# Optimization experiments

Hardware: AMD Instinct MI355X
Metric: run time of the kernel (lower is better)

## Reference

```python
import math
import jax, jax.numpy as jnp
import numpy as np

N, MA, DESIGN, RADIAL, SOFTENING, RM = 8, 24, 26, 15, 3, 5.0


def setup_inputs() -> dict:
    key = jax.random.key(0)
    k1, k2 = jax.random.split(key, 2)
    # atomic coordinates, spread out so interatomic distances are realistic (bohr)
    coords = jax.random.normal(k1, (N, MA, 3), jnp.float32) * 3.0
    # labels all >= 0 -> full padding (padding[i] == MA for every molecule)
    labels = jax.random.randint(k2, (N, MA), 0, 10)
    # deterministic synthetic Lebedev-like design (26 points on the unit sphere)
    phi = jnp.linspace(0.0, 2.0 * math.pi, DESIGN, endpoint=False).astype(jnp.float32)
    psi = jnp.linspace(0.1, math.pi - 0.1, DESIGN).astype(jnp.float32)
    sphere = jnp.stack([jnp.cos(phi) * jnp.sin(psi),
                        jnp.sin(phi) * jnp.sin(psi),
                        jnp.cos(psi)], axis=1)           # [D, 3]
    sphere_weights = jnp.full((DESIGN,), 1.0 / DESIGN, dtype=jnp.float32)
    return {"labels": labels, "coords": coords,
            "sphere": sphere, "sphere_weights": sphere_weights}


def _spheric_grid(sphere, sphere_weights):
    # Gauss-Chebyshev radial quadrature mapped by the Becke transform
    i = jnp.arange(1, RADIAL + 1, dtype=jnp.float32)
    z = -jnp.cos(math.pi * (2.0 * i - 1.0) / (2.0 * RADIAL))
    dr = 2.0 * RM * (1.0 - z) ** -2
    r = RM * (1.0 + z) / (1.0 - z)
    w = jnp.sqrt(1.0 - z ** 2) * dr * math.pi / RADIAL
    w = r ** 2 * 4.0 * math.pi * w                       # [R]
    conc = (r[:, None, None] * sphere[None]).reshape(-1, 3)          # [R*D, 3]
    wt = (sphere_weights[None, :] * w[:, None]).reshape(-1)          # [R*D]
    return conc, wt


def _becke(x, r, dm, idx):
    # x [n, mx, 3] grid points, r [n, M, 3] centers, dm [n, M, M], idx [mx]
    rx = jnp.linalg.norm(x[:, :, None, :] - r[:, None, :, :], axis=-1)   # [n, mx, M]
    # elliptic coordinate mu_ij for every grid point: [n, mx, M, M]
    mu = (rx[..., :, None] - rx[..., None, :]) / jnp.clip(dm[:, None], 1e-12, None)
    for _ in range(1, SOFTENING):                       # softening passes
        mu = 0.5 * mu * (3.0 - mu ** 2)
    mu = 0.5 * (1.0 - mu)
    mu = mu + 0.5 * jnp.eye(dm.shape[-1], dtype=x.dtype)  # diagonal -> 1
    cell = jnp.prod(mu, axis=-1)                        # [n, mx, M] cell functions
    v_i = jnp.take_along_axis(cell, idx[None, :, None], axis=2)[..., 0]
    return v_i / cell.sum(axis=2)


def reference(labels, coords, sphere, sphere_weights):
    # labels are all >= 0 here, so padding == MA for every molecule and the
    # original per-molecule loop collapses into one batched computation.
    conc, wt = _spheric_grid(sphere, sphere_weights)    # conc [ms,3], wt [ms]
    ms = conc.shape[0]
    n, M, _ = coords.shape
    dm = jnp.linalg.norm(coords[:, :, None, :] - coords[:, None, :, :], axis=-1)
    # place concentric spheres on each atom (atom-major ordering, as in torch)
    grid = (coords[:, :, None, :] + conc[None, None]).reshape(n, M * ms, 3)
    w_full = jnp.broadcast_to(wt[None, :], (M, ms)).reshape(-1)      # [M*ms]
    idx = jnp.repeat(jnp.arange(M), ms)                              # sample -> center
    v = _becke(grid, coords, dm, idx)                                # [n, M*ms]
    weights = v * w_full[None, :]
    dv = grid[:, :, None, :] - coords[:, None, :, :]                 # [n, M*ms, M, 3]
    return grid, dv, weights
```

## Files before the change

kernel.cpp:

```cpp
#include <hip/hip_runtime.h>
#include <math.h>

constexpr int MAC = 24;
constexpr int DES = 26;
constexpr int RAD = 15;
constexpr int MS  = RAD * DES;
constexpr int MX  = MAC * MS;
constexpr int PPB = 8;
constexpr int BPM = MX / PPB;

__global__ __launch_bounds__(512) void becke_precompute(
    const float* __restrict__ coords, const float* __restrict__ sphere,
    const float* __restrict__ sw, int nmol,
    float* __restrict__ inv_dm, float* __restrict__ conc4, float* __restrict__ wt)
{
    __shared__ float rr[RAD], ww[RAD];
    const int tid = threadIdx.x;
    if (tid < RAD) {
        double i   = (double)tid + 1.0;
        double z   = -cos(M_PI * (2.0 * i - 1.0) / (2.0 * (double)RAD));
        double omz = 1.0 - z;
        double dr  = 10.0 / (omz * omz);
        double r   = 5.0 * (1.0 + z) / omz;
        double w1  = sqrt(1.0 - z * z) * dr * M_PI / (double)RAD;
        rr[tid] = (float)r;
        ww[tid] = (float)(r * r * 4.0 * M_PI * w1);
    }
    __syncthreads();
    for (int t = tid; t < MS; t += 512) {
        int k = t / DES, d = t - k * DES;
        conc4[t * 4 + 0] = rr[k] * sphere[d * 3 + 0];
        conc4[t * 4 + 1] = rr[k] * sphere[d * 3 + 1];
        conc4[t * 4 + 2] = rr[k] * sphere[d * 3 + 2];
        conc4[t * 4 + 3] = 0.0f;
        wt[t] = sw[d] * ww[k];
    }
    for (int e = tid; e < nmol * MAC * MAC; e += 512) {
        int n = e / (MAC * MAC), r0 = e - n * MAC * MAC;
        int i = r0 / MAC, j = r0 - i * MAC;
        const float* cb = coords + n * MAC * 3;
        float dx = cb[i * 3 + 0] - cb[j * 3 + 0];
        float dy = cb[i * 3 + 1] - cb[j * 3 + 1];
        float dz = cb[i * 3 + 2] - cb[j * 3 + 2];
        float dd = sqrtf(dx * dx + dy * dy + dz * dz);
        inv_dm[e] = 1.0f / fmaxf(dd, 1e-12f);
    }
}

__global__ __launch_bounds__(256) void becke_main(
    const float* __restrict__ coords,
    const float* __restrict__ inv_dm,
    const float* __restrict__ conc4,
    const float* __restrict__ wt,
    float* __restrict__ og,
    float* __restrict__ odv,
    float* __restrict__ ow)
{
    const int tid = threadIdx.x;
    const int l   = tid & 31;
    const int n   = blockIdx.x / BPM;
    const int sm  = (blockIdx.x - n * BPM) * PPB + (tid >> 5);
    const int a   = sm / MS;
    const int t   = sm - a * MS;
    const bool act = (l < MAC);
    const int  i   = act ? l : (MAC - 1);

    const float4 cc  = *reinterpret_cast<const float4*>(conc4 + t * 4);
    const float  wtt = wt[t];
    const float* cb  = coords + n * MAC * 3;

    const float gx = cb[a * 3 + 0] + cc.x;
    const float gy = cb[a * 3 + 1] + cc.y;
    const float gz = cb[a * 3 + 2] + cc.z;

    const float dx = gx - cb[i * 3 + 0];
    const float dy = gy - cb[i * 3 + 1];
    const float dz = gz - cb[i * 3 + 2];
    const size_t sg = (size_t)n * MX + sm;
    if (act) {
        float* dvp = odv + (sg * MAC + i) * 3;
        dvp[0] = dx; dvp[1] = dy; dvp[2] = dz;
    }
    const float rxi = sqrtf(dx * dx + dy * dy + dz * dz);

    float inv[MAC];
    const float* irow = inv_dm + (n * MAC + i) * MAC;
    #pragma unroll
    for (int q = 0; q < MAC / 4; ++q) {
        float4 v = *reinterpret_cast<const float4*>(irow + q * 4);
        inv[q * 4 + 0] = v.x; inv[q * 4 + 1] = v.y;
        inv[q * 4 + 2] = v.z; inv[q * 4 + 3] = v.w;
    }

    float prod = 1.0f;
    #pragma unroll
    for (int j = 0; j < MAC; ++j) {
        float rxj = __shfl(rxi, j, 32);
        float mu  = (rxi - rxj) * inv[j];
        mu *= fmaf(mu * mu, -0.5f, 1.5f);
        mu *= fmaf(mu * mu, -0.5f, 1.5f);
        prod *= fmaf(mu, -0.5f, 0.5f);
    }
    float cell = act ? (prod + prod) : 0.0f;

    float sum = cell;
    #pragma unroll
    for (int m = 16; m >= 1; m >>= 1) sum += __shfl_xor(sum, m, 32);
    const float ca = __shfl(cell, a, 32);

    if (l == MAC) {
        float* gp = og + sg * 3;
        gp[0] = gx; gp[1] = gy; gp[2] = gz;
    } else if (l == MAC + 1) {
        ow[sg] = (ca / sum) * wtt;
    }
}

extern "C" void kernel_launch(void* const* d_in, const int* in_sizes, int n_in,
                              void* d_out, int out_size, void* d_ws, size_t ws_size,
                              hipStream_t stream) {
    const float* coords = (const float*)d_in[1];
    const float* sphere = (const float*)d_in[2];
    const float* sw     = (const float*)d_in[3];

    const int nmol = in_sizes[1] / (MAC * 3);

    float* ws     = (float*)d_ws;
    float* inv_dm = ws;
    float* conc4  = inv_dm + (size_t)nmol * MAC * MAC;
    float* wtab   = conc4 + MS * 4;

    float* o     = (float*)d_out;
    float* ogrid = o;
    float* odv   = ogrid + (size_t)nmol * MX * 3;
    float* owt   = odv + (size_t)nmol * MX * MAC * 3;

    becke_precompute<<<dim3(1), dim3(512), 0, stream>>>(
        coords, sphere, sw, nmol, inv_dm, conc4, wtab);
    becke_main<<<dim3(nmol * BPM), dim3(256), 0, stream>>>(
        coords, inv_dm, conc4, wtab, ogrid, odv, owt);
}
```

Measured before the change: 84.06 us.

## Process four grid points per half-warp and parallelize precompute across blocks

Each 32-lane group now handles four sample points instead of one, so the per-atom inverse-distance row and atom coordinates loaded into registers are reused across four points. Broadcasts and reductions use ds_swizzle instead of generic shuffles, and the weight normalization uses a fast reciprocal. The precompute moves from one block to a multi-block grid, packs radial weights into the conc4 w component, and pads coords to float4. This trades higher register pressure and fewer blocks for less redundant loading and less launch serialization in the precompute.

```diff
diff --git a/kernel.cpp b/kernel.cpp
--- a/kernel.cpp
+++ b/kernel.cpp
@@ -1,41 +1,42 @@
 #include <hip/hip_runtime.h>
 #include <math.h>
+#include <type_traits>
 
 constexpr int MAC = 24;
 constexpr int DES = 26;
 constexpr int RAD = 15;
 constexpr int MS  = RAD * DES;
 constexpr int MX  = MAC * MS;
-constexpr int PPB = 8;
+constexpr int PPG = 4;
+constexpr int GPB = 6;
+constexpr int PPB = PPG * GPB;
 constexpr int BPM = MX / PPB;
 
-__global__ __launch_bounds__(512) void becke_precompute(
+template <int N, int I = 0, typename F>
+__device__ __forceinline__ void static_for(F&& f) {
+    if constexpr (I < N) {
+        f(std::integral_constant<int, I>{});
+        static_for<N, I + 1>(f);
+    }
+}
+
+template <int J>
+__device__ __forceinline__ float bcast32(float v) {
+    return __int_as_float(__builtin_amdgcn_ds_swizzle(__float_as_int(v), (J << 5)));
+}
+template <int M>
+__device__ __forceinline__ float xorswz(float v) {
+    return __int_as_float(__builtin_amdgcn_ds_swizzle(__float_as_int(v), (M << 10) | 0x1f));
+}
+
+__global__ __launch_bounds__(256) void becke_pre(
     const float* __restrict__ coords, const float* __restrict__ sphere,
     const float* __restrict__ sw, int nmol,
-    float* __restrict__ inv_dm, float* __restrict__ conc4, float* __restrict__ wt)
+    float* __restrict__ inv_dm, float4* __restrict__ conc4, float4* __restrict__ cpad)
 {
-    __shared__ float rr[RAD], ww[RAD];
-    const int tid = threadIdx.x;
-    if (tid < RAD) {
-        double i   = (double)tid + 1.0;
-        double z   = -cos(M_PI * (2.0 * i - 1.0) / (2.0 * (double)RAD));
-        double omz = 1.0 - z;
-        double dr  = 10.0 / (omz * omz);
-        double r   = 5.0 * (1.0 + z) / omz;
-        double w1  = sqrt(1.0 - z * z) * dr * M_PI / (double)RAD;
-        rr[tid] = (float)r;
-        ww[tid] = (float)(r * r * 4.0 * M_PI * w1);
-    }
-    __syncthreads();
-    for (int t = tid; t < MS; t += 512) {
-        int k = t / DES, d = t - k * DES;
-        conc4[t * 4 + 0] = rr[k] * sphere[d * 3 + 0];
-        conc4[t * 4 + 1] = rr[k] * sphere[d * 3 + 1];
-        conc4[t * 4 + 2] = rr[k] * sphere[d * 3 + 2];
-        conc4[t * 4 + 3] = 0.0f;
-        wt[t] = sw[d] * ww[k];
-    }
-    for (int e = tid; e < nmol * MAC * MAC; e += 512) {
+    const int e = blockIdx.x * 256 + threadIdx.x;
+    const int nidm = nmol * MAC * MAC;
+    if (e < nidm) {
         int n = e / (MAC * MAC), r0 = e - n * MAC * MAC;
         int i = r0 / MAC, j = r0 - i * MAC;
         const float* cb = coords + n * MAC * 3;
@@ -44,75 +45,126 @@
         float dz = cb[i * 3 + 2] - cb[j * 3 + 2];
         float dd = sqrtf(dx * dx + dy * dy + dz * dz);
         inv_dm[e] = 1.0f / fmaxf(dd, 1e-12f);
+        return;
+    }
+    const int e2 = e - nidm;
+    if (e2 < MS) {
+        int k = e2 / DES, d = e2 - k * DES;
+        double i   = (double)k + 1.0;
+        double z   = -cos(M_PI * (2.0 * i - 1.0) / (2.0 * (double)RAD));
+        double omz = 1.0 - z;
+        double dr  = 10.0 / (omz * omz);
+        double r   = 5.0 * (1.0 + z) / omz;
+        double w1  = sqrt(1.0 - z * z) * dr * M_PI / (double)RAD;
+        double w   = r * r * 4.0 * M_PI * w1;
+        conc4[e2] = make_float4((float)(r * (double)sphere[d * 3 + 0]),
+                                (float)(r * (double)sphere[d * 3 + 1]),
+                                (float)(r * (double)sphere[d * 3 + 2]),
+                                (float)((double)sw[d] * w));
+        return;
+    }
+    const int e3 = e2 - MS;
+    if (e3 < nmol * MAC) {
+        cpad[e3] = make_float4(coords[e3 * 3 + 0], coords[e3 * 3 + 1],
+                               coords[e3 * 3 + 2], 0.0f);
     }
 }
 
-__global__ __launch_bounds__(256) void becke_main(
-    const float* __restrict__ coords,
-    const float* __restrict__ inv_dm,
-    const float* __restrict__ conc4,
-    const float* __restrict__ wt,
+__global__ __launch_bounds__(192) void becke_main(
+    const float4* __restrict__ cpad,
+    const float*  __restrict__ inv_dm,
+    const float4* __restrict__ conc4,
     float* __restrict__ og,
     float* __restrict__ odv,
     float* __restrict__ ow)
 {
     const int tid = threadIdx.x;
     const int l   = tid & 31;
-    const int n   = blockIdx.x / BPM;
-    const int sm  = (blockIdx.x - n * BPM) * PPB + (tid >> 5);
-    const int a   = sm / MS;
-    const int t   = sm - a * MS;
+    const int b   = blockIdx.x;
+    const int n   = b / BPM;
+    const int bm  = b - n * BPM;
+    const int s0  = bm * PPB + (tid >> 5) * PPG;
     const bool act = (l < MAC);
     const int  i   = act ? l : (MAC - 1);
 
-    const float4 cc  = *reinterpret_cast<const float4*>(conc4 + t * 4);
-    const float  wtt = wt[t];
-    const float* cb  = coords + n * MAC * 3;
+    int ap[PPG], tp[PPG];
+    #pragma unroll
+    for (int p = 0; p < PPG; ++p) {
+        int sp = s0 + p;
+        ap[p] = sp / MS;
+        tp[p] = sp - ap[p] * MS;
+    }
 
-    const float gx = cb[a * 3 + 0] + cc.x;
-    const float gy = cb[a * 3 + 1] + cc.y;
-    const float gz = cb[a * 3 + 2] + cc.z;
+    const float4 ci = cpad[n * MAC + i];
 
-    const float dx = gx - cb[i * 3 + 0];
-    const float dy = gy - cb[i * 3 + 1];
-    const float dz = gz - cb[i * 3 + 2];
-    const size_t sg = (size_t)n * MX + sm;
-    if (act) {
-        float* dvp = odv + (sg * MAC + i) * 3;
-        dvp[0] = dx; dvp[1] = dy; dvp[2] = dz;
+    float gx[PPG], gy[PPG], gz[PPG], wt[PPG];
+    #pragma unroll
+    for (int p = 0; p < PPG; ++p) {
+        float4 cc = conc4[tp[p]];
+        float4 ca = cpad[n * MAC + ap[p]];
+        gx[p] = ca.x + cc.x;
+        gy[p] = ca.y + cc.y;
+        gz[p] = ca.z + cc.z;
+        wt[p] = cc.w;
     }
-    const float rxi = sqrtf(dx * dx + dy * dy + dz * dz);
+
+    const size_t sgb = (size_t)n * MX + s0;
+
+    float rx[PPG];
+    #pragma unroll
+    for (int p = 0; p < PPG; ++p) {
+        float dx = gx[p] - ci.x;
+        float dy = gy[p] - ci.y;
+        float dz = gz[p] - ci.z;
+        if (act) {
+            float* dvp = odv + ((sgb + p) * MAC + i) * 3;
+            dvp[0] = dx; dvp[1] = dy; dvp[2] = dz;
+        }
+        rx[p] = sqrtf(dx * dx + dy * dy + dz * dz);
+    }
 
     float inv[MAC];
-    const float* irow = inv_dm + (n * MAC + i) * MAC;
-    #pragma unroll
-    for (int q = 0; q < MAC / 4; ++q) {
-        float4 v = *reinterpret_cast<const float4*>(irow + q * 4);
-        inv[q * 4 + 0] = v.x; inv[q * 4 + 1] = v.y;
-        inv[q * 4 + 2] = v.z; inv[q * 4 + 3] = v.w;
+    {
+        const float* irow = inv_dm + (n * MAC + i) * MAC;
+        #pragma unroll
+        for (int q = 0; q < MAC / 4; ++q) {
+            float4 v = *reinterpret_cast<const float4*>(irow + q * 4);
+            inv[q * 4 + 0] = v.x; inv[q * 4 + 1] = v.y;
+            inv[q * 4 + 2] = v.z; inv[q * 4 + 3] = v.w;
+        }
     }
 
-    float prod = 1.0f;
+    float prod[PPG] = {1.0f, 1.0f, 1.0f, 1.0f};
+    static_for<MAC>([&](auto jc) {
+        constexpr int j = jc.value;
+        const float aj = inv[j];
+        #pragma unroll
+        for (int p = 0; p < PPG; ++p) {
+            float rj = bcast32<j>(rx[p]);
+            float mu = (rx[p] - rj) * aj;
+            mu *= fmaf(mu * mu, -0.5f, 1.5f);
+            mu *= fmaf(mu * mu, -0.5f, 1.5f);
+            prod[p] *= fmaf(mu, -0.5f, 0.5f);
+        }
+    });
+
     #pragma unroll
-    for (int j = 0; j < MAC; ++j) {
-        float rxj = __shfl(rxi, j, 32);
-        float mu  = (rxi - rxj) * inv[j];
-        mu *= fmaf(mu * mu, -0.5f, 1.5f);
-        mu *= fmaf(mu * mu, -0.5f, 1.5f);
-        prod *= fmaf(mu, -0.5f, 0.5f);
+    for (int p = 0; p < PPG; ++p) {
+        float cell = act ? (prod[p] + prod[p]) : 0.0f;
+        float sum = cell;
+        sum += xorswz<1>(sum);
+        sum += xorswz<2>(sum);
+        sum += xorswz<4>(sum);
+        sum += xorswz<8>(sum);
+        sum += xorswz<16>(sum);
+        if (l == ap[p])
+            ow[sgb + p] = cell * __builtin_amdgcn_rcpf(sum) * wt[p];
     }
-    float cell = act ? (prod + prod) : 0.0f;
 
-    float sum = cell;
-    #pragma unroll
-    for (int m = 16; m >= 1; m >>= 1) sum += __shfl_xor(sum, m, 32);
-    const float ca = __shfl(cell, a, 32);
-
-    if (l == MAC) {
-        float* gp = og + sg * 3;
-        gp[0] = gx; gp[1] = gy; gp[2] = gz;
-    } else if (l == MAC + 1) {
-        ow[sg] = (ca / sum) * wtt;
+    if (l >= MAC && l < MAC + PPG) {
+        int p = l - MAC;
+        float* gp = og + (sgb + p) * 3;
+        gp[0] = gx[p]; gp[1] = gy[p]; gp[2] = gz[p];
     }
 }
 
@@ -125,18 +177,21 @@
 
     const int nmol = in_sizes[1] / (MAC * 3);
 
-    float* ws     = (float*)d_ws;
-    float* inv_dm = ws;
-    float* conc4  = inv_dm + (size_t)nmol * MAC * MAC;
-    float* wtab   = conc4 + MS * 4;
+    float*  ws     = (float*)d_ws;
+    float*  inv_dm = ws;
+    float4* conc4  = (float4*)(inv_dm + (size_t)nmol * MAC * MAC);
+    float4* cpad   = conc4 + MS;
 
     float* o     = (float*)d_out;
     float* ogrid = o;
     float* odv   = ogrid + (size_t)nmol * MX * 3;
     float* owt   = odv + (size_t)nmol * MX * MAC * 3;
 
-    becke_precompute<<<dim3(1), dim3(512), 0, stream>>>(
-        coords, sphere, sw, nmol, inv_dm, conc4, wtab);
-    becke_main<<<dim3(nmol * BPM), dim3(256), 0, stream>>>(
-        coords, inv_dm, conc4, wtab, ogrid, odv, owt);
+    const int pre_elems  = nmol * MAC * MAC + MS + nmol * MAC;
+    const int pre_blocks = (pre_elems + 255) / 256;
+    becke_pre<<<dim3(pre_blocks), dim3(256), 0, stream>>>(
+        coords, sphere, sw, nmol, inv_dm, conc4, cpad);
+
+    becke_main<<<dim3(nmol * BPM), dim3(192), 0, stream>>>(
+        cpad, inv_dm, conc4, ogrid, odv, owt);
 }
```

Result: slower. 87.94 us (+4.6%).
